# Kernel tuning notes

Hardware: AMD Instinct MI355X
Metric: run time of the kernel (lower is better)

## Reference

```python
import jax, jax.numpy as jnp
import numpy as np

EPS = 1e-5

def sage_conv(x, edge_index, w_l, b_l, w_r):
    # PyG SAGEConv with mean aggregation: lin_l(mean of source-neighbor feats per dst) + lin_r(x)
    n = x.shape[0]
    src, dst = edge_index[0], edge_index[1]
    agg = jax.ops.segment_sum(x[src], dst, num_segments=n)  # [N, d]
    deg = jax.ops.segment_sum(jnp.ones((edge_index.shape[1],), x.dtype), dst, num_segments=n)
    agg = agg / jnp.maximum(deg, 1.0)[:, None]
    return agg @ w_l + b_l + x @ w_r

def batchnorm_eval(x, gamma, beta, mean, var):
    return (x - mean) * (gamma * jax.lax.rsqrt(var + EPS)) + beta

def setup_inputs() -> dict:
    key = jax.random.key(0)
    ks = jax.random.split(key, 12)
    N, E, D, H, O = 10000, 160000, 512, 512, 256
    inp = {
        'x': jax.random.normal(ks[0], (N, D), jnp.float32),
        'edge_index': jax.random.randint(ks[1], (2, E), 0, N, jnp.int32),
        'w_l1': jax.random.normal(ks[2], (D, H), jnp.float32) * (1.0 / np.sqrt(D)),
        'b1': jnp.zeros((H,), jnp.float32),
        'w_r1': jax.random.normal(ks[3], (D, H), jnp.float32) * (1.0 / np.sqrt(D)),
        'bn1_gamma': jnp.ones((H,), jnp.float32),
        'bn1_beta': jnp.zeros((H,), jnp.float32),
        'bn1_mean': jax.random.normal(ks[4], (H,), jnp.float32) * 0.1,
        'bn1_var': jax.random.uniform(ks[5], (H,), jnp.float32, 0.5, 1.5),
        'w_l2': jax.random.normal(ks[6], (H, H), jnp.float32) * (1.0 / np.sqrt(H)),
        'b2': jnp.zeros((H,), jnp.float32),
        'w_r2': jax.random.normal(ks[7], (H, H), jnp.float32) * (1.0 / np.sqrt(H)),
        'bn2_gamma': jnp.ones((H,), jnp.float32),
        'bn2_beta': jnp.zeros((H,), jnp.float32),
        'bn2_mean': jax.random.normal(ks[8], (H,), jnp.float32) * 0.1,
        'bn2_var': jax.random.uniform(ks[9], (H,), jnp.float32, 0.5, 1.5),
        'w_l3': jax.random.normal(ks[10], (H, O), jnp.float32) * (1.0 / np.sqrt(H)),
        'b3': jnp.zeros((O,), jnp.float32),
        'w_r3': jax.random.normal(ks[11], (H, O), jnp.float32) * (1.0 / np.sqrt(H)),
    }
    return inp

def reference(x, edge_index, w_l1, b1, w_r1, bn1_gamma, bn1_beta, bn1_mean, bn1_var,
              w_l2, b2, w_r2, bn2_gamma, bn2_beta, bn2_mean, bn2_var,
              w_l3, b3, w_r3):
    # Layer 1: SAGEConv -> BN (eval) -> ReLU (dropout is identity in eval)
    h = sage_conv(x, edge_index, w_l1, b1, w_r1)
    h = jax.nn.relu(batchnorm_eval(h, bn1_gamma, bn1_beta, bn1_mean, bn1_var))
    # Layer 2
    h = sage_conv(h, edge_index, w_l2, b2, w_r2)
    h = jax.nn.relu(batchnorm_eval(h, bn2_gamma, bn2_beta, bn2_mean, bn2_var))
    # Layer 3 (no BN/ReLU)
    return sage_conv(h, edge_index, w_l3, b3, w_r3)
```

## Files before the change

kernel.cpp:

```cpp
#include <hip/hip_runtime.h>

#define NNODE 10000
#define NEDGE 160000

using frag8 = __attribute__((ext_vector_type(8))) short;
using f32x4 = __attribute__((ext_vector_type(4))) float;

__device__ __forceinline__ unsigned short f2bf(float f) {
    union { float f; unsigned u; } v; v.f = f;
    unsigned r = (v.u + 0x7fffu + ((v.u >> 16) & 1u)) >> 16;
    return (unsigned short)r;
}
__device__ __forceinline__ float bf2f(unsigned short s) {
    union { unsigned u; float f; } v; v.u = ((unsigned)s) << 16; return v.f;
}

__global__ __launch_bounds__(1024) void k_scan(const int* __restrict__ deg,
                                               int* __restrict__ rs,
                                               int* __restrict__ cur, int n, int total) {
    const int tid = threadIdx.x;
    const int CH = 10;
    const int base = tid * CH;
    int vals[CH];
    int tsum = 0;
#pragma unroll
    for (int j = 0; j < CH; j++) {
        int v = (base + j < n) ? deg[base + j] : 0;
        vals[j] = v; tsum += v;
    }
    const int lane = tid & 63, wid = tid >> 6;
    int x = tsum;
#pragma unroll
    for (int d = 1; d < 64; d <<= 1) {
        int y = __shfl_up(x, d, 64);
        if (lane >= d) x += y;
    }
    __shared__ int wt[16];
    if (lane == 63) wt[wid] = x;
    __syncthreads();
    if (tid == 0) {
        int c = 0;
#pragma unroll
        for (int k = 0; k < 16; k++) { int t = wt[k]; wt[k] = c; c += t; }
    }
    __syncthreads();
    int run = wt[wid] + x - tsum;
#pragma unroll
    for (int j = 0; j < CH; j++) {
        if (base + j < n) { rs[base + j] = run; cur[base + j] = run; }
        run += vals[j];
    }
    if (tid == 0) rs[n] = total;
}

__global__ void k_fill(const int* __restrict__ src, const int* __restrict__ dst,
                       int E, int* __restrict__ cur, int* __restrict__ csr) {
    int e = blockIdx.x * 256 + threadIdx.x;
    if (e < E) {
        int p = atomicAdd(&cur[dst[e]], 1);
        csr[p] = src[e];
    }
}

__global__ __launch_bounds__(256) void k_prep(
    const float* __restrict__ x, unsigned short* __restrict__ xb,
    const float* __restrict__ wl1, const float* __restrict__ wr1,
    const float* __restrict__ wl2, const float* __restrict__ wr2,
    const float* __restrict__ wl3, const float* __restrict__ wr3,
    unsigned short* __restrict__ bt1, unsigned short* __restrict__ bt2,
    unsigned short* __restrict__ bt3,
    const float* __restrict__ b1, const float* __restrict__ g1, const float* __restrict__ be1,
    const float* __restrict__ m1, const float* __restrict__ v1,
    const float* __restrict__ b2, const float* __restrict__ g2, const float* __restrict__ be2,
    const float* __restrict__ m2, const float* __restrict__ v2,
    const float* __restrict__ b3,
    float* __restrict__ sc1, float* __restrict__ sh1,
    float* __restrict__ sc2, float* __restrict__ sh2,
    float* __restrict__ sc3, float* __restrict__ sh3,
    const int* __restrict__ dstI, int* __restrict__ deg) {
    const int b = blockIdx.x, tid = threadIdx.x;
    if (b < 5000) {
        int i = b * 256 + tid;
        float4 f = ((const float4*)x)[i];
        ushort4 o;
        o.x = f2bf(f.x); o.y = f2bf(f.y); o.z = f2bf(f.z); o.w = f2bf(f.w);
        ((ushort4*)xb)[i] = o;
        return;
    }
    if (b >= 6281) {
        int e = (b - 6281) * 256 + tid;
        if (e < NEDGE) atomicAdd(&deg[dstI[e]], 1);
        return;
    }
    if (b == 6280) {
        for (int t = tid; t < 512; t += 256) {
            float s1 = g1[t] * rsqrtf(v1[t] + 1e-5f);
            sc1[t] = s1; sh1[t] = (b1[t] - m1[t]) * s1 + be1[t];
            float s2 = g2[t] * rsqrtf(v2[t] + 1e-5f);
            sc2[t] = s2; sh2[t] = (b2[t] - m2[t]) * s2 + be2[t];
        }
        if (tid < 256) { sc3[tid] = 1.0f; sh3[tid] = b3[tid]; }
        return;
    }
    __shared__ float t[32][33];
    int tj = b - 5000;
    const float* srcp; unsigned short* dstp; int C, koff, ntilesN;
    if (tj < 1024) {
        int job = tj >> 8; int tile = tj & 255; C = 512; ntilesN = 16;
        srcp = (job == 0) ? wl1 : (job == 1) ? wr1 : (job == 2) ? wl2 : wr2;
        dstp = (job < 2) ? bt1 : bt2; koff = (job & 1) * 512;
        tj = tile;
    } else {
        int jj = tj - 1024; int job = jj >> 7; int tile = jj & 127; C = 256; ntilesN = 8;
        srcp = (job == 0) ? wl3 : wr3; dstp = bt3; koff = job * 512;
        tj = tile;
    }
    int k0 = (tj / ntilesN) * 32, c0 = (tj % ntilesN) * 32;
    int tx = tid & 31, ty = tid >> 5;
#pragma unroll
    for (int q = 0; q < 4; q++)
        t[ty + 8 * q][tx] = srcp[(long)(k0 + ty + 8 * q) * C + c0 + tx];
    __syncthreads();
#pragma unroll
    for (int q = 0; q < 4; q++)
        dstp[(long)(c0 + ty + 8 * q) * 1024 + koff + k0 + tx] = f2bf(t[tx][ty + 8 * q]);
}

__global__ __launch_bounds__(64) void k_agg(const unsigned short* __restrict__ S,
                                            const int* __restrict__ rs, const int* __restrict__ csr,
                                            unsigned short* __restrict__ outb) {
    const int n = blockIdx.x;
    const int c = blockIdx.y * 256 + threadIdx.x * 4;
    const int s = rs[n], e = rs[n + 1];
    float a0 = 0.f, a1 = 0.f, a2 = 0.f, a3 = 0.f;
    int i = s;
    for (; i + 4 <= e; i += 4) {
        int r0 = csr[i], r1 = csr[i + 1], r2 = csr[i + 2], r3 = csr[i + 3];
        uint2 u0 = *(const uint2*)(S + (long)r0 * 512 + c);
        uint2 u1 = *(const uint2*)(S + (long)r1 * 512 + c);
        uint2 u2 = *(const uint2*)(S + (long)r2 * 512 + c);
        uint2 u3 = *(const uint2*)(S + (long)r3 * 512 + c);
        a0 += bf2f((unsigned short)(u0.x & 0xffffu)); a1 += bf2f((unsigned short)(u0.x >> 16));
        a2 += bf2f((unsigned short)(u0.y & 0xffffu)); a3 += bf2f((unsigned short)(u0.y >> 16));
        a0 += bf2f((unsigned short)(u1.x & 0xffffu)); a1 += bf2f((unsigned short)(u1.x >> 16));
        a2 += bf2f((unsigned short)(u1.y & 0xffffu)); a3 += bf2f((unsigned short)(u1.y >> 16));
        a0 += bf2f((unsigned short)(u2.x & 0xffffu)); a1 += bf2f((unsigned short)(u2.x >> 16));
        a2 += bf2f((unsigned short)(u2.y & 0xffffu)); a3 += bf2f((unsigned short)(u2.y >> 16));
        a0 += bf2f((unsigned short)(u3.x & 0xffffu)); a1 += bf2f((unsigned short)(u3.x >> 16));
        a2 += bf2f((unsigned short)(u3.y & 0xffffu)); a3 += bf2f((unsigned short)(u3.y >> 16));
    }
    for (; i < e; i++) {
        uint2 u = *(const uint2*)(S + (long)csr[i] * 512 + c);
        a0 += bf2f((unsigned short)(u.x & 0xffffu)); a1 += bf2f((unsigned short)(u.x >> 16));
        a2 += bf2f((unsigned short)(u.y & 0xffffu)); a3 += bf2f((unsigned short)(u.y >> 16));
    }
    const int cnt = e - s;
    const float inv = 1.f / (float)(cnt > 1 ? cnt : 1);
    uint2 o;
    o.x = (unsigned)f2bf(a0 * inv) | ((unsigned)f2bf(a1 * inv) << 16);
    o.y = (unsigned)f2bf(a2 * inv) | ((unsigned)f2bf(a3 * inv) << 16);
    *(uint2*)(outb + (long)n * 512 + c) = o;
}

template <int MODE, int NOUT>
__global__ __launch_bounds__(256, 2) void k_gemm(const unsigned short* __restrict__ Agg,
                                                 const unsigned short* __restrict__ Self,
                                                 const unsigned short* __restrict__ Bt,
                                                 const float* __restrict__ sc, const float* __restrict__ sh,
                                                 unsigned short* __restrict__ hout, float* __restrict__ fout,
                                                 int M) {
    constexpr int NT = NOUT / 128;
    constexpr int QSH = (NT == 4) ? 5 : 4;
    const int b = blockIdx.x;
    const int X = b & 7;
    const int q = (b >> 3) & (NT - 1);
    const int g = b >> QSH;
    const int m0 = (g * 8 + X) * 128;
    if (m0 >= M) return;
    const int n0 = q * 128;

    __shared__ __align__(16) short As[2][128 * 64];
    __shared__ __align__(16) short Bs[2][128 * 64];
    const int tid = threadIdx.x;
    const int w = tid >> 6, lane = tid & 63;
    const int wm = (w >> 1) * 64, wn = (w & 1) * 64;
    const int fr = lane & 15, fq = lane >> 4, sw = fr & 7;
    const int srow = w * 8 + (lane >> 3);
    const int scol = (((lane & 7) ^ (lane >> 3)) * 8);
    const int ldsOff = w * 8 * 64;

    f32x4 acc[4][4];
#pragma unroll
    for (int i = 0; i < 4; i++)
#pragma unroll
        for (int j = 0; j < 4; j++)
#pragma unroll
            for (int r = 0; r < 4; r++) acc[i][j][r] = 0.f;

    auto issue = [&](int t, int buf) {
        const short* abase = (const short*)((t < 8) ? Agg : Self);
        const int kk = (t & 7) * 64;
        const int k0 = t * 64;
#pragma unroll
        for (int cch = 0; cch < 4; cch++) {
            __builtin_amdgcn_global_load_lds(
                (const __attribute__((address_space(1))) void*)(abase + (long)(m0 + cch * 32 + srow) * 512 + kk + scol),
                (__attribute__((address_space(3))) void*)(&As[buf][ldsOff + cch * 32 * 64]), 16, 0, 0);
            __builtin_amdgcn_global_load_lds(
                (const __attribute__((address_space(1))) void*)((const short*)Bt + (long)(n0 + cch * 32 + srow) * 1024 + k0 + scol),
                (__attribute__((address_space(3))) void*)(&Bs[buf][ldsOff + cch * 32 * 64]), 16, 0, 0);
        }
    };

    issue(0, 0);
#pragma unroll
    for (int t = 0; t < 16; t++) {
        const int cur = t & 1;
        __syncthreads();
        if (t < 15) issue(t + 1, cur ^ 1);
#pragma unroll
        for (int ks = 0; ks < 2; ks++) {
            frag8 af[4], bf[4];
#pragma unroll
            for (int i = 0; i < 4; i++)
                af[i] = *(const frag8*)(&As[cur][(wm + i * 16 + fr) * 64 + (((ks * 4 + fq) ^ sw) * 8)]);
#pragma unroll
            for (int j = 0; j < 4; j++)
                bf[j] = *(const frag8*)(&Bs[cur][(wn + j * 16 + fr) * 64 + (((ks * 4 + fq) ^ sw) * 8)]);
#pragma unroll
            for (int i = 0; i < 4; i++)
#pragma unroll
                for (int j = 0; j < 4; j++)
                    acc[i][j] = __builtin_amdgcn_mfma_f32_16x16x32_bf16(af[i], bf[j], acc[i][j], 0, 0, 0);
        }
    }

    float scj[4], shj[4];
#pragma unroll
    for (int j = 0; j < 4; j++) {
        int col = n0 + wn + j * 16 + fr;
        scj[j] = sc[col]; shj[j] = sh[col];
    }
#pragma unroll
    for (int i = 0; i < 4; i++) {
        int rowb = m0 + wm + i * 16 + fq * 4;
#pragma unroll
        for (int j = 0; j < 4; j++) {
            int col = n0 + wn + j * 16 + fr;
#pragma unroll
            for (int r = 0; r < 4; r++) {
                int row = rowb + r;
                if (row < M) {
                    float y = acc[i][j][r] * scj[j] + shj[j];
                    if constexpr (MODE == 0) {
                        y = fmaxf(y, 0.f);
                        hout[(long)row * 512 + col] = f2bf(y);
                    } else {
                        fout[(long)row * NOUT + col] = y;
                    }
                }
            }
        }
    }
}

extern "C" void kernel_launch(void* const* d_in, const int* in_sizes, int n_in,
                              void* d_out, int out_size, void* d_ws, size_t ws_size,
                              hipStream_t stream) {
    const float* x    = (const float*)d_in[0];
    const int*   ei   = (const int*)d_in[1];
    const float* w_l1 = (const float*)d_in[2];
    const float* b1   = (const float*)d_in[3];
    const float* w_r1 = (const float*)d_in[4];
    const float* g1   = (const float*)d_in[5];
    const float* be1  = (const float*)d_in[6];
    const float* m1   = (const float*)d_in[7];
    const float* v1   = (const float*)d_in[8];
    const float* w_l2 = (const float*)d_in[9];
    const float* b2   = (const float*)d_in[10];
    const float* w_r2 = (const float*)d_in[11];
    const float* g2   = (const float*)d_in[12];
    const float* be2  = (const float*)d_in[13];
    const float* m2   = (const float*)d_in[14];
    const float* v2   = (const float*)d_in[15];
    const float* w_l3 = (const float*)d_in[16];
    const float* b3   = (const float*)d_in[17];
    const float* w_r3 = (const float*)d_in[18];
    float* out = (float*)d_out;

    const int N = NNODE, E = NEDGE;
    const int* srcI = ei;
    const int* dstI = ei + E;

    char* w = (char*)d_ws;
    auto alloc = [&](size_t bytes) { void* p = (void*)w; w += (bytes + 255) & ~(size_t)255; return p; };
    int* deg = (int*)alloc((size_t)N * 4);
    int* rs  = (int*)alloc((size_t)(N + 1) * 4);
    int* cur = (int*)alloc((size_t)N * 4);
    int* csr = (int*)alloc((size_t)E * 4);
    unsigned short* xb   = (unsigned short*)alloc((size_t)N * 512 * 2);
    unsigned short* bt1  = (unsigned short*)alloc((size_t)512 * 1024 * 2);
    unsigned short* bt2  = (unsigned short*)alloc((size_t)512 * 1024 * 2);
    unsigned short* bt3  = (unsigned short*)alloc((size_t)256 * 1024 * 2);
    float* sc1 = (float*)alloc(512 * 4); float* sh1 = (float*)alloc(512 * 4);
    float* sc2 = (float*)alloc(512 * 4); float* sh2 = (float*)alloc(512 * 4);
    float* sc3 = (float*)alloc(256 * 4); float* sh3 = (float*)alloc(256 * 4);
    unsigned short* agg_a = (unsigned short*)alloc((size_t)N * 512 * 2);
    unsigned short* h1    = (unsigned short*)alloc((size_t)N * 512 * 2);
    unsigned short* h2    = (unsigned short*)alloc((size_t)N * 512 * 2);
    (void)alloc(256 * 1024);

    hipMemsetAsync(deg, 0, (size_t)N * 4, stream);
    k_prep<<<6906, 256, 0, stream>>>(x, xb, w_l1, w_r1, w_l2, w_r2, w_l3, w_r3,
                                     bt1, bt2, bt3,
                                     b1, g1, be1, m1, v1, b2, g2, be2, m2, v2, b3,
                                     sc1, sh1, sc2, sh2, sc3, sh3, dstI, deg);
    k_scan<<<1, 1024, 0, stream>>>(deg, rs, cur, N, E);
    k_fill<<<(E + 255) / 256, 256, 0, stream>>>(srcI, dstI, E, cur, csr);

    dim3 ga(N, 2);

    k_agg<<<ga, 64, 0, stream>>>(xb, rs, csr, agg_a);
    k_gemm<0, 512><<<320, 256, 0, stream>>>(agg_a, xb, bt1, sc1, sh1, h1, nullptr, N);
    k_agg<<<ga, 64, 0, stream>>>(h1, rs, csr, agg_a);
    k_gemm<0, 512><<<320, 256, 0, stream>>>(agg_a, h1, bt2, sc2, sh2, h2, nullptr, N);
    k_agg<<<ga, 64, 0, stream>>>(h2, rs, csr, agg_a);
    k_gemm<1, 256><<<160, 256, 0, stream>>>(agg_a, h2, bt3, sc3, sh3, nullptr, out, N);
}
```

Measured before the change: 253.8 us.

## Reorder layer-3 to transform-then-aggregate and widen aggregation loads

Layer 3 now multiplies h2 by the concatenated [W_l3 | W_r3] first, producing a 512-wide bf16 PQ matrix. A fused kernel then mean-aggregates the 256-wide projected P half over neighbors and adds the Q half plus bias, which halves the gathered width for the last layer. The aggregation kernel uses one 64-thread block per node with 16-byte loads instead of two blocks with 8-byte loads. The GEMM epilogue swaps MFMA operands so each lane writes four contiguous columns as one packed store. Storing the intermediate projection in bf16 before aggregation adds rounding error.

New measurement: 245.6 us. 1.03x faster.

```diff
diff --git a/kernel.cpp b/kernel.cpp
--- a/kernel.cpp
+++ b/kernel.cpp
@@ -98,21 +98,21 @@
             sc1[t] = s1; sh1[t] = (b1[t] - m1[t]) * s1 + be1[t];
             float s2 = g2[t] * rsqrtf(v2[t] + 1e-5f);
             sc2[t] = s2; sh2[t] = (b2[t] - m2[t]) * s2 + be2[t];
-        }
-        if (tid < 256) { sc3[tid] = 1.0f; sh3[tid] = b3[tid]; }
+            sc3[t] = 1.0f; sh3[t] = (t < 256) ? 0.0f : b3[t - 256];
+        }
         return;
     }
     __shared__ float t[32][33];
     int tj = b - 5000;
-    const float* srcp; unsigned short* dstp; int C, koff, ntilesN;
+    const float* srcp; unsigned short* dstp; int C, koff, ntilesN, rowoff, dstride;
     if (tj < 1024) {
         int job = tj >> 8; int tile = tj & 255; C = 512; ntilesN = 16;
         srcp = (job == 0) ? wl1 : (job == 1) ? wr1 : (job == 2) ? wl2 : wr2;
-        dstp = (job < 2) ? bt1 : bt2; koff = (job & 1) * 512;
+        dstp = (job < 2) ? bt1 : bt2; koff = (job & 1) * 512; rowoff = 0; dstride = 1024;
         tj = tile;
     } else {
         int jj = tj - 1024; int job = jj >> 7; int tile = jj & 127; C = 256; ntilesN = 8;
-        srcp = (job == 0) ? wl3 : wr3; dstp = bt3; koff = job * 512;
+        srcp = (job == 0) ? wl3 : wr3; dstp = bt3; koff = 0; rowoff = job * 256; dstride = 512;
         tj = tile;
     }
     int k0 = (tj / ntilesN) * 32, c0 = (tj % ntilesN) * 32;
@@ -123,54 +123,92 @@
     __syncthreads();
 #pragma unroll
     for (int q = 0; q < 4; q++)
-        dstp[(long)(c0 + ty + 8 * q) * 1024 + koff + k0 + tx] = f2bf(t[tx][ty + 8 * q]);
+        dstp[(long)(rowoff + c0 + ty + 8 * q) * dstride + koff + k0 + tx] = f2bf(t[tx][ty + 8 * q]);
 }
 
 __global__ __launch_bounds__(64) void k_agg(const unsigned short* __restrict__ S,
                                             const int* __restrict__ rs, const int* __restrict__ csr,
                                             unsigned short* __restrict__ outb) {
     const int n = blockIdx.x;
-    const int c = blockIdx.y * 256 + threadIdx.x * 4;
+    const int c = threadIdx.x * 8;
     const int s = rs[n], e = rs[n + 1];
+    float a[8];
+#pragma unroll
+    for (int k = 0; k < 8; k++) a[k] = 0.f;
+    int i = s;
+    for (; i + 4 <= e; i += 4) {
+        int r0 = csr[i], r1 = csr[i + 1], r2 = csr[i + 2], r3 = csr[i + 3];
+        uint4 u0 = *(const uint4*)(S + (long)r0 * 512 + c);
+        uint4 u1 = *(const uint4*)(S + (long)r1 * 512 + c);
+        uint4 u2 = *(const uint4*)(S + (long)r2 * 512 + c);
+        uint4 u3 = *(const uint4*)(S + (long)r3 * 512 + c);
+#define ACC(u) \
+        a[0] += bf2f((unsigned short)((u).x & 0xffffu)); a[1] += bf2f((unsigned short)((u).x >> 16)); \
+        a[2] += bf2f((unsigned short)((u).y & 0xffffu)); a[3] += bf2f((unsigned short)((u).y >> 16)); \
+        a[4] += bf2f((unsigned short)((u).z & 0xffffu)); a[5] += bf2f((unsigned short)((u).z >> 16)); \
+        a[6] += bf2f((unsigned short)((u).w & 0xffffu)); a[7] += bf2f((unsigned short)((u).w >> 16));
+        ACC(u0) ACC(u1) ACC(u2) ACC(u3)
+    }
+    for (; i < e; i++) {
+        uint4 u = *(const uint4*)(S + (long)csr[i] * 512 + c);
+        ACC(u)
+    }
+#undef ACC
+    const int cnt = e - s;
+    const float inv = 1.f / (float)(cnt > 1 ? cnt : 1);
+    uint4 o;
+    o.x = (unsigned)f2bf(a[0] * inv) | ((unsigned)f2bf(a[1] * inv) << 16);
+    o.y = (unsigned)f2bf(a[2] * inv) | ((unsigned)f2bf(a[3] * inv) << 16);
+    o.z = (unsigned)f2bf(a[4] * inv) | ((unsigned)f2bf(a[5] * inv) << 16);
+    o.w = (unsigned)f2bf(a[6] * inv) | ((unsigned)f2bf(a[7] * inv) << 16);
+    *(uint4*)(outb + (long)n * 512 + c) = o;
+}
+
+__global__ __launch_bounds__(64) void k_agg_fuse(const unsigned short* __restrict__ PQ,
+                                                 const int* __restrict__ rs, const int* __restrict__ csr,
+                                                 float* __restrict__ out) {
+    const int n = blockIdx.x;
+    const int c = threadIdx.x * 4;
+    const int s = rs[n], e = rs[n + 1];
+    uint2 q = *(const uint2*)(PQ + (long)n * 512 + 256 + c);
     float a0 = 0.f, a1 = 0.f, a2 = 0.f, a3 = 0.f;
     int i = s;
     for (; i + 4 <= e; i += 4) {
         int r0 = csr[i], r1 = csr[i + 1], r2 = csr[i + 2], r3 = csr[i + 3];
-        uint2 u0 = *(const uint2*)(S + (long)r0 * 512 + c);
-        uint2 u1 = *(const uint2*)(S + (long)r1 * 512 + c);
-        uint2 u2 = *(const uint2*)(S + (long)r2 * 512 + c);
-        uint2 u3 = *(const uint2*)(S + (long)r3 * 512 + c);
-        a0 += bf2f((unsigned short)(u0.x & 0xffffu)); a1 += bf2f((unsigned short)(u0.x >> 16));
-        a2 += bf2f((unsigned short)(u0.y & 0xffffu)); a3 += bf2f((unsigned short)(u0.y >> 16));
-        a0 += bf2f((unsigned short)(u1.x & 0xffffu)); a1 += bf2f((unsigned short)(u1.x >> 16));
-        a2 += bf2f((unsigned short)(u1.y & 0xffffu)); a3 += bf2f((unsigned short)(u1.y >> 16));
-        a0 += bf2f((unsigned short)(u2.x & 0xffffu)); a1 += bf2f((unsigned short)(u2.x >> 16));
-        a2 += bf2f((unsigned short)(u2.y & 0xffffu)); a3 += bf2f((unsigned short)(u2.y >> 16));
-        a0 += bf2f((unsigned short)(u3.x & 0xffffu)); a1 += bf2f((unsigned short)(u3.x >> 16));
-        a2 += bf2f((unsigned short)(u3.y & 0xffffu)); a3 += bf2f((unsigned short)(u3.y >> 16));
+        uint2 u0 = *(const uint2*)(PQ + (long)r0 * 512 + c);
+        uint2 u1 = *(const uint2*)(PQ + (long)r1 * 512 + c);
+        uint2 u2 = *(const uint2*)(PQ + (long)r2 * 512 + c);
+        uint2 u3 = *(const uint2*)(PQ + (long)r3 * 512 + c);
+#define ACC(u) \
+        a0 += bf2f((unsigned short)((u).x & 0xffffu)); a1 += bf2f((unsigned short)((u).x >> 16)); \
+        a2 += bf2f((unsigned short)((u).y & 0xffffu)); a3 += bf2f((unsigned short)((u).y >> 16));
+        ACC(u0) ACC(u1) ACC(u2) ACC(u3)
     }
     for (; i < e; i++) {
-        uint2 u = *(const uint2*)(S + (long)csr[i] * 512 + c);
-        a0 += bf2f((unsigned short)(u.x & 0xffffu)); a1 += bf2f((unsigned short)(u.x >> 16));
-        a2 += bf2f((unsigned short)(u.y & 0xffffu)); a3 += bf2f((unsigned short)(u.y >> 16));
-    }
+        uint2 u = *(const uint2*)(PQ + (long)csr[i] * 512 + c);
+        ACC(u)
+    }
+#undef ACC
     const int cnt = e - s;
     const float inv = 1.f / (float)(cnt > 1 ? cnt : 1);
-    uint2 o;
-    o.x = (unsigned)f2bf(a0 * inv) | ((unsigned)f2bf(a1 * inv) << 16);
-    o.y = (unsigned)f2bf(a2 * inv) | ((unsigned)f2bf(a3 * inv) << 16);
-    *(uint2*)(outb + (long)n * 512 + c) = o;
-}
-
-template <int MODE, int NOUT>
+    float4 o;
+    o.x = a0 * inv + bf2f((unsigned short)(q.x & 0xffffu));
+    o.y = a1 * inv + bf2f((unsigned short)(q.x >> 16));
+    o.z = a2 * inv + bf2f((unsigned short)(q.y & 0xffffu));
+    o.w = a3 * inv + bf2f((unsigned short)(q.y >> 16));
+    *(float4*)&out[(long)n * 256 + c] = o;
+}
+
+template <int MODE, int NOUT, bool SPLIT>
 __global__ __launch_bounds__(256, 2) void k_gemm(const unsigned short* __restrict__ Agg,
                                                  const unsigned short* __restrict__ Self,
                                                  const unsigned short* __restrict__ Bt,
                                                  const float* __restrict__ sc, const float* __restrict__ sh,
-                                                 unsigned short* __restrict__ hout, float* __restrict__ fout,
-                                                 int M) {
+                                                 unsigned short* __restrict__ hout, int M) {
     constexpr int NT = NOUT / 128;
     constexpr int QSH = (NT == 4) ? 5 : 4;
+    constexpr int KSTEPS = SPLIT ? 16 : 8;
+    constexpr int BSTR = SPLIT ? 1024 : 512;
     const int b = blockIdx.x;
     const int X = b & 7;
     const int q = (b >> 3) & (NT - 1);
@@ -198,8 +236,15 @@
             for (int r = 0; r < 4; r++) acc[i][j][r] = 0.f;
 
     auto issue = [&](int t, int buf) {
-        const short* abase = (const short*)((t < 8) ? Agg : Self);
-        const int kk = (t & 7) * 64;
+        const short* abase;
+        int kk;
+        if constexpr (SPLIT) {
+            abase = (const short*)((t < 8) ? Agg : Self);
+            kk = (t & 7) * 64;
+        } else {
+            abase = (const short*)Self;
+            kk = t * 64;
+        }
         const int k0 = t * 64;
 #pragma unroll
         for (int cch = 0; cch < 4; cch++) {
@@ -207,17 +252,17 @@
                 (const __attribute__((address_space(1))) void*)(abase + (long)(m0 + cch * 32 + srow) * 512 + kk + scol),
                 (__attribute__((address_space(3))) void*)(&As[buf][ldsOff + cch * 32 * 64]), 16, 0, 0);
             __builtin_amdgcn_global_load_lds(
-                (const __attribute__((address_space(1))) void*)((const short*)Bt + (long)(n0 + cch * 32 + srow) * 1024 + k0 + scol),
+                (const __attribute__((address_space(1))) void*)((const short*)Bt + (long)(n0 + cch * 32 + srow) * BSTR + k0 + scol),
                 (__attribute__((address_space(3))) void*)(&Bs[buf][ldsOff + cch * 32 * 64]), 16, 0, 0);
         }
     };
 
     issue(0, 0);
 #pragma unroll
-    for (int t = 0; t < 16; t++) {
+    for (int t = 0; t < KSTEPS; t++) {
         const int cur = t & 1;
         __syncthreads();
-        if (t < 15) issue(t + 1, cur ^ 1);
+        if (t < KSTEPS - 1) issue(t + 1, cur ^ 1);
 #pragma unroll
         for (int ks = 0; ks < 2; ks++) {
             frag8 af[4], bf[4];
@@ -231,34 +276,31 @@
             for (int i = 0; i < 4; i++)
 #pragma unroll
                 for (int j = 0; j < 4; j++)
-                    acc[i][j] = __builtin_amdgcn_mfma_f32_16x16x32_bf16(af[i], bf[j], acc[i][j], 0, 0, 0);
-        }
-    }
-
-    float scj[4], shj[4];
+                    acc[i][j] = __builtin_amdgcn_mfma_f32_16x16x32_bf16(bf[j], af[i], acc[i][j], 0, 0, 0);
+        }
+    }
+
 #pragma unroll
     for (int j = 0; j < 4; j++) {
-        int col = n0 + wn + j * 16 + fr;
-        scj[j] = sc[col]; shj[j] = sh[col];
-    }
-#pragma unroll
-    for (int i = 0; i < 4; i++) {
-        int rowb = m0 + wm + i * 16 + fq * 4;
-#pragma unroll
-        for (int j = 0; j < 4; j++) {
-            int col = n0 + wn + j * 16 + fr;
-#pragma unroll
-            for (int r = 0; r < 4; r++) {
-                int row = rowb + r;
-                if (row < M) {
-                    float y = acc[i][j][r] * scj[j] + shj[j];
-                    if constexpr (MODE == 0) {
-                        y = fmaxf(y, 0.f);
-                        hout[(long)row * 512 + col] = f2bf(y);
-                    } else {
-                        fout[(long)row * NOUT + col] = y;
-                    }
+        const int colb = n0 + wn + j * 16 + fq * 4;
+        const float4 s4 = *(const float4*)&sc[colb];
+        const float4 h4 = *(const float4*)&sh[colb];
+#pragma unroll
+        for (int i = 0; i < 4; i++) {
+            const int row = m0 + wm + i * 16 + fr;
+            if (row < M) {
+                float y0 = acc[i][j][0] * s4.x + h4.x;
+                float y1 = acc[i][j][1] * s4.y + h4.y;
+                float y2 = acc[i][j][2] * s4.z + h4.z;
+                float y3 = acc[i][j][3] * s4.w + h4.w;
+                if constexpr (MODE == 0) {
+                    y0 = fmaxf(y0, 0.f); y1 = fmaxf(y1, 0.f);
+                    y2 = fmaxf(y2, 0.f); y3 = fmaxf(y3, 0.f);
                 }
+                uint2 o;
+                o.x = (unsigned)f2bf(y0) | ((unsigned)f2bf(y1) << 16);
+                o.y = (unsigned)f2bf(y2) | ((unsigned)f2bf(y3) << 16);
+                *(uint2*)&hout[(long)row * NOUT + colb] = o;
             }
         }
     }
@@ -301,10 +343,10 @@
     unsigned short* xb   = (unsigned short*)alloc((size_t)N * 512 * 2);
     unsigned short* bt1  = (unsigned short*)alloc((size_t)512 * 1024 * 2);
     unsigned short* bt2  = (unsigned short*)alloc((size_t)512 * 1024 * 2);
-    unsigned short* bt3  = (unsigned short*)alloc((size_t)256 * 1024 * 2);
+    unsigned short* bt3  = (unsigned short*)alloc((size_t)512 * 512 * 2);
     float* sc1 = (float*)alloc(512 * 4); float* sh1 = (float*)alloc(512 * 4);
     float* sc2 = (float*)alloc(512 * 4); float* sh2 = (float*)alloc(512 * 4);
-    float* sc3 = (float*)alloc(256 * 4); float* sh3 = (float*)alloc(256 * 4);
+    float* sc3 = (float*)alloc(512 * 4); float* sh3 = (float*)alloc(512 * 4);
     unsigned short* agg_a = (unsigned short*)alloc((size_t)N * 512 * 2);
     unsigned short* h1    = (unsigned short*)alloc((size_t)N * 512 * 2);
     unsigned short* h2    = (unsigned short*)alloc((size_t)N * 512 * 2);
@@ -318,12 +360,10 @@
     k_scan<<<1, 1024, 0, stream>>>(deg, rs, cur, N, E);
     k_fill<<<(E + 255) / 256, 256, 0, stream>>>(srcI, dstI, E, cur, csr);
 
-    dim3 ga(N, 2);
-
-    k_agg<<<ga, 64, 0, stream>>>(xb, rs, csr, agg_a);
-    k_gemm<0, 512><<<320, 256, 0, stream>>>(agg_a, xb, bt1, sc1, sh1, h1, nullptr, N);
-    k_agg<<<ga, 64, 0, stream>>>(h1, rs, csr, agg_a);
-    k_gemm<0, 512><<<320, 256, 0, stream>>>(agg_a, h1, bt2, sc2, sh2, h2, nullptr, N);
-    k_agg<<<ga, 64, 0, stream>>>(h2, rs, csr, agg_a);
-    k_gemm<1, 256><<<160, 256, 0, stream>>>(agg_a, h2, bt3, sc3, sh3, nullptr, out, N);
-}
+    k_agg<<<N, 64, 0, stream>>>(xb, rs, csr, agg_a);
+    k_gemm<0, 512, true><<<320, 256, 0, stream>>>(agg_a, xb, bt1, sc1, sh1, h1, N);
+    k_agg<<<N, 64, 0, stream>>>(h1, rs, csr, agg_a);
+    k_gemm<0, 512, true><<<320, 256, 0, stream>>>(agg_a, h1, bt2, sc2, sh2, h2, N);
+    k_gemm<2, 512, false><<<320, 256, 0, stream>>>(h2, h2, bt3, sc3, sh3, agg_a, N);
+    k_agg_fuse<<<N, 64, 0, stream>>>(agg_a, rs, csr, out);
+}
```

## Transform features before aggregation and fuse BN/ReLU epilogue into aggregation kernel

Applied to the files above, without the earlier changes.

Uses linearity of the mean to multiply each node's features by [W_l | W_r] first. This yields a PQ buffer of width 2*out, and the kernel then averages the projected neighbour rows P and adds the self term Q, with BN scale/shift and ReLU fused into the aggregation. The GEMM becomes a single K=512 product with a smaller M tile and a bf16 store. Aggregation gathers projected rows, which for layer 3 are narrower (256), and uses 4 nodes per 256-thread block. In exchange, P is rounded to bf16 before averaging, which shifts numerics, and the GEMM now writes a wider intermediate.

After: 252.1 us. About the same (-0.7%).

```diff
diff --git a/kernel.cpp b/kernel.cpp
--- a/kernel.cpp
+++ b/kernel.cpp
@@ -98,21 +98,21 @@
             sc1[t] = s1; sh1[t] = (b1[t] - m1[t]) * s1 + be1[t];
             float s2 = g2[t] * rsqrtf(v2[t] + 1e-5f);
             sc2[t] = s2; sh2[t] = (b2[t] - m2[t]) * s2 + be2[t];
-        }
-        if (tid < 256) { sc3[tid] = 1.0f; sh3[tid] = b3[tid]; }
+            if (t < 256) { sc3[t] = 1.0f; sh3[t] = b3[t]; }
+        }
         return;
     }
     __shared__ float t[32][33];
     int tj = b - 5000;
-    const float* srcp; unsigned short* dstp; int C, koff, ntilesN;
+    const float* srcp; unsigned short* dstp; int C, ntilesN, rowoff;
     if (tj < 1024) {
         int job = tj >> 8; int tile = tj & 255; C = 512; ntilesN = 16;
         srcp = (job == 0) ? wl1 : (job == 1) ? wr1 : (job == 2) ? wl2 : wr2;
-        dstp = (job < 2) ? bt1 : bt2; koff = (job & 1) * 512;
+        dstp = (job < 2) ? bt1 : bt2; rowoff = (job & 1) * 512;
         tj = tile;
     } else {
         int jj = tj - 1024; int job = jj >> 7; int tile = jj & 127; C = 256; ntilesN = 8;
-        srcp = (job == 0) ? wl3 : wr3; dstp = bt3; koff = job * 512;
+        srcp = (job == 0) ? wl3 : wr3; dstp = bt3; rowoff = job * 256;
         tj = tile;
     }
     int k0 = (tj / ntilesN) * 32, c0 = (tj % ntilesN) * 32;
@@ -123,142 +123,174 @@
     __syncthreads();
 #pragma unroll
     for (int q = 0; q < 4; q++)
-        dstp[(long)(c0 + ty + 8 * q) * 1024 + koff + k0 + tx] = f2bf(t[tx][ty + 8 * q]);
-}
-
-__global__ __launch_bounds__(64) void k_agg(const unsigned short* __restrict__ S,
-                                            const int* __restrict__ rs, const int* __restrict__ csr,
-                                            unsigned short* __restrict__ outb) {
-    const int n = blockIdx.x;
-    const int c = blockIdx.y * 256 + threadIdx.x * 4;
+        dstp[(long)(rowoff + c0 + ty + 8 * q) * 512 + k0 + tx] = f2bf(t[tx][ty + 8 * q]);
+}
+
+template <int W, bool RELU, bool F32OUT>
+__global__ __launch_bounds__(256) void k_aggf(const unsigned short* __restrict__ PQ,
+                                              const int* __restrict__ rs, const int* __restrict__ csr,
+                                              const float* __restrict__ sc, const float* __restrict__ sh,
+                                              unsigned short* __restrict__ hout, float* __restrict__ fout) {
+    constexpr int NV = W / 64;
+    constexpr int PQW = 2 * W;
+    const int n = blockIdx.x * 4 + (threadIdx.x >> 6);
+    const int lane = threadIdx.x & 63;
+    const int c = lane * NV;
     const int s = rs[n], e = rs[n + 1];
-    float a0 = 0.f, a1 = 0.f, a2 = 0.f, a3 = 0.f;
+    float a[NV];
+#pragma unroll
+    for (int k = 0; k < NV; k++) a[k] = 0.f;
+
+    float qv[NV], scv[NV], shv[NV];
+    {
+        const unsigned short* qp = PQ + (long)n * PQW + W + c;
+#pragma unroll
+        for (int k = 0; k < NV; k += 4) {
+            uint2 u = *(const uint2*)(qp + k);
+            qv[k + 0] = bf2f((unsigned short)(u.x & 0xffffu));
+            qv[k + 1] = bf2f((unsigned short)(u.x >> 16));
+            qv[k + 2] = bf2f((unsigned short)(u.y & 0xffffu));
+            qv[k + 3] = bf2f((unsigned short)(u.y >> 16));
+            float4 s4 = *(const float4*)&sc[c + k];
+            float4 h4 = *(const float4*)&sh[c + k];
+            scv[k + 0] = s4.x; scv[k + 1] = s4.y; scv[k + 2] = s4.z; scv[k + 3] = s4.w;
+            shv[k + 0] = h4.x; shv[k + 1] = h4.y; shv[k + 2] = h4.z; shv[k + 3] = h4.w;
+        }
+    }
+
+#define ACC4(p) { \
+        uint2 u = *(const uint2*)((p)); \
+        a[K + 0] += bf2f((unsigned short)(u.x & 0xffffu)); \
+        a[K + 1] += bf2f((unsigned short)(u.x >> 16)); \
+        a[K + 2] += bf2f((unsigned short)(u.y & 0xffffu)); \
+        a[K + 3] += bf2f((unsigned short)(u.y >> 16)); }
+
     int i = s;
     for (; i + 4 <= e; i += 4) {
         int r0 = csr[i], r1 = csr[i + 1], r2 = csr[i + 2], r3 = csr[i + 3];
-        uint2 u0 = *(const uint2*)(S + (long)r0 * 512 + c);
-        uint2 u1 = *(const uint2*)(S + (long)r1 * 512 + c);
-        uint2 u2 = *(const uint2*)(S + (long)r2 * 512 + c);
-        uint2 u3 = *(const uint2*)(S + (long)r3 * 512 + c);
-        a0 += bf2f((unsigned short)(u0.x & 0xffffu)); a1 += bf2f((unsigned short)(u0.x >> 16));
-        a2 += bf2f((unsigned short)(u0.y & 0xffffu)); a3 += bf2f((unsigned short)(u0.y >> 16));
-        a0 += bf2f((unsigned short)(u1.x & 0xffffu)); a1 += bf2f((unsigned short)(u1.x >> 16));
-        a2 += bf2f((unsigned short)(u1.y & 0xffffu)); a3 += bf2f((unsigned short)(u1.y >> 16));
-        a0 += bf2f((unsigned short)(u2.x & 0xffffu)); a1 += bf2f((unsigned short)(u2.x >> 16));
-        a2 += bf2f((unsigned short)(u2.y & 0xffffu)); a3 += bf2f((unsigned short)(u2.y >> 16));
-        a0 += bf2f((unsigned short)(u3.x & 0xffffu)); a1 += bf2f((unsigned short)(u3.x >> 16));
-        a2 += bf2f((unsigned short)(u3.y & 0xffffu)); a3 += bf2f((unsigned short)(u3.y >> 16));
+        const unsigned short* p0 = PQ + (long)r0 * PQW + c;
+        const unsigned short* p1 = PQ + (long)r1 * PQW + c;
+        const unsigned short* p2 = PQ + (long)r2 * PQW + c;
+        const unsigned short* p3 = PQ + (long)r3 * PQW + c;
+#pragma unroll
+        for (int K = 0; K < NV; K += 4) {
+            ACC4(p0 + K) ACC4(p1 + K) ACC4(p2 + K) ACC4(p3 + K)
+        }
     }
     for (; i < e; i++) {
-        uint2 u = *(const uint2*)(S + (long)csr[i] * 512 + c);
-        a0 += bf2f((unsigned short)(u.x & 0xffffu)); a1 += bf2f((unsigned short)(u.x >> 16));
-        a2 += bf2f((unsigned short)(u.y & 0xffffu)); a3 += bf2f((unsigned short)(u.y >> 16));
-    }
+        const unsigned short* p = PQ + (long)csr[i] * PQW + c;
+#pragma unroll
+        for (int K = 0; K < NV; K += 4) ACC4(p + K)
+    }
+#undef ACC4
+
     const int cnt = e - s;
     const float inv = 1.f / (float)(cnt > 1 ? cnt : 1);
-    uint2 o;
-    o.x = (unsigned)f2bf(a0 * inv) | ((unsigned)f2bf(a1 * inv) << 16);
-    o.y = (unsigned)f2bf(a2 * inv) | ((unsigned)f2bf(a3 * inv) << 16);
-    *(uint2*)(outb + (long)n * 512 + c) = o;
-}
-
-template <int MODE, int NOUT>
-__global__ __launch_bounds__(256, 2) void k_gemm(const unsigned short* __restrict__ Agg,
-                                                 const unsigned short* __restrict__ Self,
+    float y[NV];
+#pragma unroll
+    for (int k = 0; k < NV; k++) {
+        y[k] = (a[k] * inv + qv[k]) * scv[k] + shv[k];
+        if constexpr (RELU) y[k] = fmaxf(y[k], 0.f);
+    }
+    if constexpr (F32OUT) {
+#pragma unroll
+        for (int k = 0; k < NV; k += 4) {
+            float4 o; o.x = y[k]; o.y = y[k + 1]; o.z = y[k + 2]; o.w = y[k + 3];
+            *(float4*)&fout[(long)n * W + c + k] = o;
+        }
+    } else {
+#pragma unroll
+        for (int k = 0; k < NV; k += 4) {
+            uint2 o;
+            o.x = (unsigned)f2bf(y[k]) | ((unsigned)f2bf(y[k + 1]) << 16);
+            o.y = (unsigned)f2bf(y[k + 2]) | ((unsigned)f2bf(y[k + 3]) << 16);
+            *(uint2*)&hout[(long)n * W + c + k] = o;
+        }
+    }
+}
+
+template <int NOUT>
+__global__ __launch_bounds__(256, 2) void k_gemm(const unsigned short* __restrict__ A,
                                                  const unsigned short* __restrict__ Bt,
-                                                 const float* __restrict__ sc, const float* __restrict__ sh,
-                                                 unsigned short* __restrict__ hout, float* __restrict__ fout,
-                                                 int M) {
+                                                 unsigned short* __restrict__ hout, int M) {
     constexpr int NT = NOUT / 128;
-    constexpr int QSH = (NT == 4) ? 5 : 4;
+    constexpr int QSH = (NT == 8) ? 6 : 5;
     const int b = blockIdx.x;
     const int X = b & 7;
     const int q = (b >> 3) & (NT - 1);
     const int g = b >> QSH;
-    const int m0 = (g * 8 + X) * 128;
+    const int m0 = (g * 8 + X) * 64;
     if (m0 >= M) return;
     const int n0 = q * 128;
 
-    __shared__ __align__(16) short As[2][128 * 64];
+    __shared__ __align__(16) short As[2][64 * 64];
     __shared__ __align__(16) short Bs[2][128 * 64];
     const int tid = threadIdx.x;
     const int w = tid >> 6, lane = tid & 63;
-    const int wm = (w >> 1) * 64, wn = (w & 1) * 64;
+    const int wm = (w >> 1) * 32, wn = (w & 1) * 64;
     const int fr = lane & 15, fq = lane >> 4, sw = fr & 7;
     const int srow = w * 8 + (lane >> 3);
     const int scol = (((lane & 7) ^ (lane >> 3)) * 8);
     const int ldsOff = w * 8 * 64;
 
-    f32x4 acc[4][4];
-#pragma unroll
-    for (int i = 0; i < 4; i++)
+    f32x4 acc[2][4];
+#pragma unroll
+    for (int i = 0; i < 2; i++)
 #pragma unroll
         for (int j = 0; j < 4; j++)
 #pragma unroll
             for (int r = 0; r < 4; r++) acc[i][j][r] = 0.f;
 
     auto issue = [&](int t, int buf) {
-        const short* abase = (const short*)((t < 8) ? Agg : Self);
-        const int kk = (t & 7) * 64;
         const int k0 = t * 64;
+#pragma unroll
+        for (int cch = 0; cch < 2; cch++) {
+            __builtin_amdgcn_global_load_lds(
+                (const __attribute__((address_space(1))) void*)((const short*)A + (long)(m0 + cch * 32 + srow) * 512 + k0 + scol),
+                (__attribute__((address_space(3))) void*)(&As[buf][ldsOff + cch * 32 * 64]), 16, 0, 0);
+        }
 #pragma unroll
         for (int cch = 0; cch < 4; cch++) {
             __builtin_amdgcn_global_load_lds(
-                (const __attribute__((address_space(1))) void*)(abase + (long)(m0 + cch * 32 + srow) * 512 + kk + scol),
-                (__attribute__((address_space(3))) void*)(&As[buf][ldsOff + cch * 32 * 64]), 16, 0, 0);
-            __builtin_amdgcn_global_load_lds(
-                (const __attribute__((address_space(1))) void*)((const short*)Bt + (long)(n0 + cch * 32 + srow) * 1024 + k0 + scol),
+                (const __attribute__((address_space(1))) void*)((const short*)Bt + (long)(n0 + cch * 32 + srow) * 512 + k0 + scol),
                 (__attribute__((address_space(3))) void*)(&Bs[buf][ldsOff + cch * 32 * 64]), 16, 0, 0);
         }
     };
 
     issue(0, 0);
 #pragma unroll
-    for (int t = 0; t < 16; t++) {
+    for (int t = 0; t < 8; t++) {
         const int cur = t & 1;
         __syncthreads();
-        if (t < 15) issue(t + 1, cur ^ 1);
+        if (t < 7) issue(t + 1, cur ^ 1);
 #pragma unroll
         for (int ks = 0; ks < 2; ks++) {
-            frag8 af[4], bf[4];
-#pragma unroll
-            for (int i = 0; i < 4; i++)
+            frag8 af[2], bf[4];
+#pragma unroll
+            for (int i = 0; i < 2; i++)
                 af[i] = *(const frag8*)(&As[cur][(wm + i * 16 + fr) * 64 + (((ks * 4 + fq) ^ sw) * 8)]);
 #pragma unroll
             for (int j = 0; j < 4; j++)
                 bf[j] = *(const frag8*)(&Bs[cur][(wn + j * 16 + fr) * 64 + (((ks * 4 + fq) ^ sw) * 8)]);
 #pragma unroll
-            for (int i = 0; i < 4; i++)
+            for (int i = 0; i < 2; i++)
 #pragma unroll
                 for (int j = 0; j < 4; j++)
-                    acc[i][j] = __builtin_amdgcn_mfma_f32_16x16x32_bf16(af[i], bf[j], acc[i][j], 0, 0, 0);
-        }
-    }
-
-    float scj[4], shj[4];
+                    acc[i][j] = __builtin_amdgcn_mfma_f32_16x16x32_bf16(bf[j], af[i], acc[i][j], 0, 0, 0);
+        }
+    }
+
 #pragma unroll
     for (int j = 0; j < 4; j++) {
-        int col = n0 + wn + j * 16 + fr;
-        scj[j] = sc[col]; shj[j] = sh[col];
-    }
-#pragma unroll
-    for (int i = 0; i < 4; i++) {
-        int rowb = m0 + wm + i * 16 + fq * 4;
-#pragma unroll
-        for (int j = 0; j < 4; j++) {
-            int col = n0 + wn + j * 16 + fr;
-#pragma unroll
-            for (int r = 0; r < 4; r++) {
-                int row = rowb + r;
-                if (row < M) {
-                    float y = acc[i][j][r] * scj[j] + shj[j];
-                    if constexpr (MODE == 0) {
-                        y = fmaxf(y, 0.f);
-                        hout[(long)row * 512 + col] = f2bf(y);
-                    } else {
-                        fout[(long)row * NOUT + col] = y;
-                    }
-                }
+        const int colb = n0 + wn + j * 16 + fq * 4;
+#pragma unroll
+        for (int i = 0; i < 2; i++) {
+            const int row = m0 + wm + i * 16 + fr;
+            if (row < M) {
+                uint2 o;
+                o.x = (unsigned)f2bf(acc[i][j][0]) | ((unsigned)f2bf(acc[i][j][1]) << 16);
+                o.y = (unsigned)f2bf(acc[i][j][2]) | ((unsigned)f2bf(acc[i][j][3]) << 16);
+                *(uint2*)&hout[(long)row * NOUT + colb] = o;
             }
         }
     }
@@ -299,15 +331,15 @@
     int* cur = (int*)alloc((size_t)N * 4);
     int* csr = (int*)alloc((size_t)E * 4);
     unsigned short* xb   = (unsigned short*)alloc((size_t)N * 512 * 2);
-    unsigned short* bt1  = (unsigned short*)alloc((size_t)512 * 1024 * 2);
-    unsigned short* bt2  = (unsigned short*)alloc((size_t)512 * 1024 * 2);
-    unsigned short* bt3  = (unsigned short*)alloc((size_t)256 * 1024 * 2);
+    unsigned short* bt1  = (unsigned short*)alloc((size_t)1024 * 512 * 2);
+    unsigned short* bt2  = (unsigned short*)alloc((size_t)1024 * 512 * 2);
+    unsigned short* bt3  = (unsigned short*)alloc((size_t)512 * 512 * 2);
     float* sc1 = (float*)alloc(512 * 4); float* sh1 = (float*)alloc(512 * 4);
     float* sc2 = (float*)alloc(512 * 4); float* sh2 = (float*)alloc(512 * 4);
     float* sc3 = (float*)alloc(256 * 4); float* sh3 = (float*)alloc(256 * 4);
-    unsigned short* agg_a = (unsigned short*)alloc((size_t)N * 512 * 2);
-    unsigned short* h1    = (unsigned short*)alloc((size_t)N * 512 * 2);
-    unsigned short* h2    = (unsigned short*)alloc((size_t)N * 512 * 2);
+    unsigned short* PQ = (unsigned short*)alloc((size_t)N * 1024 * 2);
+    unsigned short* h1 = (unsigned short*)alloc((size_t)N * 512 * 2);
+    unsigned short* h2 = (unsigned short*)alloc((size_t)N * 512 * 2);
     (void)alloc(256 * 1024);
 
     hipMemsetAsync(deg, 0, (size_t)N * 4, stream);
@@ -318,12 +350,10 @@
     k_scan<<<1, 1024, 0, stream>>>(deg, rs, cur, N, E);
     k_fill<<<(E + 255) / 256, 256, 0, stream>>>(srcI, dstI, E, cur, csr);
 
-    dim3 ga(N, 2);
-
-    k_agg<<<ga, 64, 0, stream>>>(xb, rs, csr, agg_a);
-    k_gemm<0, 512><<<320, 256, 0, stream>>>(agg_a, xb, bt1, sc1, sh1, h1, nullptr, N);
-    k_agg<<<ga, 64, 0, stream>>>(h1, rs, csr, agg_a);
-    k_gemm<0, 512><<<320, 256, 0, stream>>>(agg_a, h1, bt2, sc2, sh2, h2, nullptr, N);
-    k_agg<<<ga, 64, 0, stream>>>(h2, rs, csr, agg_a);
-    k_gemm<1, 256><<<160, 256, 0, stream>>>(agg_a, h2, bt3, sc3, sh3, nullptr, out, N);
-}
+    k_gemm<1024><<<1280, 256, 0, stream>>>(xb, bt1, PQ, N);
+    k_aggf<512, true, false><<<2500, 256, 0, stream>>>(PQ, rs, csr, sc1, sh1, h1, nullptr);
+    k_gemm<1024><<<1280, 256, 0, stream>>>(h1, bt2, PQ, N);
+    k_aggf<512, true, false><<<2500, 256, 0, stream>>>(PQ, rs, csr, sc2, sh2, h2, nullptr);
+    k_gemm<512><<<640, 256, 0, stream>>>(h2, bt3, PQ, N);
+    k_aggf<256, false, true><<<2500, 256, 0, stream>>>(PQ, rs, csr, sc3, sh3, nullptr, out);
+}
```
